# Kernel optimization log

Hardware: AMD Instinct MI355X
Metric: run time of the kernel (lower is better)

## Reference

```python
import jax, jax.numpy as jnp
import numpy as np

B, L, DM, NL, ED, NS, DC, RK, CD, Q = 8, 1024, 256, 4, 512, 16, 4, 16, 64, 2


def _ln(x, g, b, eps=1e-5):
    m = x.mean(-1, keepdims=True)
    v = ((x - m) ** 2).mean(-1, keepdims=True)
    return (x - m) / jnp.sqrt(v + eps) * g + b


def setup_inputs() -> dict:
    key = jax.random.key(0)
    ks = jax.random.split(key, 32)
    rn = lambda k, sh, s=0.02: jax.random.normal(k, sh, jnp.float32) * s
    inp = {
        "tokens": jax.random.randint(ks[0], (B, L), 0, Q),
        "T": jax.random.uniform(ks[1], (B,), jnp.float32, 0.5, 2.0),
        "tok_embed": rn(ks[2], (Q, DM)),
        "pos_embed": rn(ks[3], (L, DM)),
        "tw1": rn(ks[4], (1, CD), 0.5),
        "tb1": rn(ks[5], (CD,), 0.1),
        "tw2": rn(ks[6], (CD, CD), 0.1),
        "tb2": rn(ks[7], (CD,), 0.1),
        "ag": jnp.ones((NL, DM), jnp.float32),
        "ab": jnp.zeros((NL, DM), jnp.float32),
        "apw": rn(ks[8], (NL, CD, 2 * DM), 0.01),
        "apb": jnp.zeros((NL, 2 * DM), jnp.float32),
        "in_w": rn(ks[9], (NL, DM, 2 * ED)),
        "conv_w": rn(ks[10], (NL, ED, DC), 0.2),
        "conv_b": jnp.zeros((NL, ED), jnp.float32),
        "xp_w": rn(ks[11], (NL, ED, RK + 2 * NS)),
        "dt_w": rn(ks[12], (NL, RK, ED), 0.1),
        "dt_b": rn(ks[13], (NL, ED), 0.1) - 4.0,  # softplus(~-4) gives small dt
        "A_log": jnp.log(jnp.broadcast_to(jnp.arange(1, NS + 1, dtype=jnp.float32), (NL, ED, NS))),
        "Dp": jnp.ones((NL, ED), jnp.float32),
        "out_w": rn(ks[14], (NL, ED, DM)),
        "fg": jnp.ones((DM,), jnp.float32),
        "fb": jnp.zeros((DM,), jnp.float32),
        "hw": rn(ks[15], (DM, Q)),
        "hb": jnp.zeros((Q,), jnp.float32),
    }
    return inp


def reference(tokens, T, tok_embed, pos_embed, tw1, tb1, tw2, tb2, ag, ab, apw, apb,
              in_w, conv_w, conv_b, xp_w, dt_w, dt_b, A_log, Dp, out_w, fg, fb, hw, hb):
    b, l = tokens.shape
    # shift-right token embedding + positional embedding
    emb = tok_embed[tokens]                                   # [B,L,DM]
    x = jnp.concatenate([jnp.zeros((b, 1, emb.shape[-1]), emb.dtype), emb[:, :-1]], axis=1)
    x = x + pos_embed[:l]
    # temperature conditioning MLP (exact GELU as in torch nn.GELU)
    h = jax.nn.gelu(T[:, None] @ tw1 + tb1, approximate=False)
    cond = h @ tw2 + tb2                                      # [B,CD]

    def comb(e1, e2):
        a1, b1 = e1
        a2, b2 = e2
        return a1 * a2, a2 * b1 + b2

    for i in range(NL):
        # AdaLN: (1 + scale) * LN(x) + shift
        ss = cond @ apw[i] + apb[i]                           # [B,2*DM]
        sc, sh = ss[:, :DM], ss[:, DM:]
        xn = (1.0 + sc[:, None, :]) * _ln(x, ag[i], ab[i]) + sh[:, None, :]
        # MambaBlock
        xz = xn @ in_w[i]                                     # [B,L,2*ED]
        xs, z = xz[..., :ED], xz[..., ED:]
        # causal depthwise conv1d (left-pad d_conv-1)
        xc = jnp.transpose(xs, (0, 2, 1))                     # [B,ED,L]
        xc = jax.lax.conv_general_dilated(xc, conv_w[i][:, None, :], (1,), [(DC - 1, 0)],
                                          feature_group_count=ED)
        xc = xc + conv_b[i][None, :, None]
        xs = jax.nn.silu(jnp.transpose(xc, (0, 2, 1)))        # [B,L,ED]
        # input-dependent SSM params
        xd = xs @ xp_w[i]                                     # [B,L,RK+2*NS]
        dlt = jax.nn.softplus(xd[..., :RK] @ dt_w[i] + dt_b[i])  # [B,L,ED]
        Bm, Cm = xd[..., RK:RK + NS], xd[..., RK + NS:]       # [B,L,NS]
        A = -jnp.exp(A_log[i])                                # [ED,NS]
        dA = jnp.exp(dlt[..., None] * A)                      # [B,L,ED,NS]
        dBx = (dlt * xs)[..., None] * Bm[:, :, None, :]       # [B,L,ED,NS]
        # selective scan: h_t = dA_t * h_{t-1} + dBx_t (parallel associative scan)
        _, hs = jax.lax.associative_scan(comb, (dA, dBx), axis=1)
        y = jnp.einsum('blen,bln->ble', hs, Cm) + Dp[i] * xs
        y = y * jax.nn.silu(z)
        x = x + y @ out_w[i]

    x = _ln(x, fg, fb)
    return x @ hw + hb                                        # [B,L,Q]
```

## Files before the change

### kernel.cpp

```cpp
#include <hip/hip_runtime.h>
#include <hip/hip_bf16.h>
#include <math.h>

#define B_   8
#define L_   1024
#define DM_  256
#define NL_  4
#define ED_  512
#define NS_  16
#define DC_  4
#define RK_  16
#define CD_  64
#define Q_   2

#define SEG_  32
#define SLEN_ 32

typedef __hip_bfloat16 bf16_t;
typedef __attribute__((ext_vector_type(8))) short short8;
typedef __attribute__((ext_vector_type(4))) float floatx4;

__device__ __forceinline__ float geluf(float x) {
    return 0.5f * x * (1.0f + erff(x * 0.70710678118654752f));
}
__device__ __forceinline__ float siluf(float x) {
    return x / (1.0f + __expf(-x));
}
__device__ __forceinline__ float softplusf(float x) {
    return (x > 20.0f) ? x : log1pf(expf(x));
}
__device__ __forceinline__ float b2f(bf16_t v) { return __bfloat162float(v); }
__device__ __forceinline__ short f2bfbits(float v) {
    return __builtin_bit_cast(short, __float2bfloat16(v));
}

__global__ void k_transpose_all(const float* __restrict__ in_w,
                                const float* __restrict__ xp_w,
                                const float* __restrict__ out_w,
                                bf16_t* __restrict__ in_wT,
                                bf16_t* __restrict__ xp_wT,
                                bf16_t* __restrict__ out_wT) {
    __shared__ float t[32][33];
    int z = blockIdx.z;
    int which = z >> 2, layer = z & 3;
    const float* src; bf16_t* dst; int R, C;
    if (which == 0)      { R = DM_; C = 2 * ED_; src = in_w;  dst = in_wT;  }
    else if (which == 1) { R = ED_; C = 48;      src = xp_w;  dst = xp_wT;  }
    else                 { R = ED_; C = DM_;     src = out_w; dst = out_wT; }
    src += (size_t)layer * R * C;
    dst += (size_t)layer * R * C;
    int c0 = blockIdx.x * 32, r0 = blockIdx.y * 32;
    if (c0 >= C || r0 >= R) return;
    int tx = threadIdx.x & 31, ty = threadIdx.x >> 5;
    #pragma unroll
    for (int i = 0; i < 32; i += 8) {
        int r = r0 + ty + i, c = c0 + tx;
        t[ty + i][tx] = (r < R && c < C) ? src[(size_t)r * C + c] : 0.f;
    }
    __syncthreads();
    #pragma unroll
    for (int i = 0; i < 32; i += 8) {
        int c = c0 + ty + i, r = r0 + tx;
        if (c < C && r < R) dst[(size_t)c * R + r] = __float2bfloat16(t[tx][ty + i]);
    }
}

__global__ void k_embed(const int* __restrict__ tokens,
                        const float* __restrict__ tok_embed,
                        const float* __restrict__ pos_embed,
                        float* __restrict__ x) {
    int row = blockIdx.x;
    int d = threadIdx.x;
    int b = row / L_, l = row % L_;
    float v = pos_embed[l * DM_ + d];
    if (l > 0) {
        int tok = tokens[b * L_ + l - 1];
        v += tok_embed[tok * DM_ + d];
    }
    x[row * DM_ + d] = v;
}

__global__ void k_prep(const float* __restrict__ T,
                       const float* __restrict__ tw1, const float* __restrict__ tb1,
                       const float* __restrict__ tw2, const float* __restrict__ tb2,
                       const float* __restrict__ apw, const float* __restrict__ apb,
                       float* __restrict__ ss) {
    __shared__ float h[CD_], cnd[CD_];
    int b = blockIdx.x, layer = blockIdx.y;
    int j = threadIdx.x;
    if (j < CD_) h[j] = geluf(T[b] * tw1[j] + tb1[j]);
    __syncthreads();
    if (j < CD_) {
        float acc = tb2[j];
        #pragma unroll
        for (int c = 0; c < CD_; c++) acc += h[c] * tw2[c * CD_ + j];
        cnd[j] = acc;
    }
    __syncthreads();
    const float* w = apw + (size_t)layer * CD_ * 2 * DM_;
    float acc = apb[layer * 2 * DM_ + j];
    #pragma unroll
    for (int c = 0; c < CD_; c++) acc += cnd[c] * w[c * 2 * DM_ + j];
    ss[((size_t)layer * B_ + b) * 2 * DM_ + j] = acc;
}

__global__ __launch_bounds__(256) void k_ln_gemm_in(
        const float* __restrict__ x,
        const float* __restrict__ ag, const float* __restrict__ ab,
        const float* __restrict__ ss,
        const bf16_t* __restrict__ Bt,
        bf16_t* __restrict__ xz, int layer) {
    constexpr int BM = 64, BN = 128, K = 256, N = 2 * ED_;
    constexpr int TM = 2, TN = 4;
    __shared__ __align__(16) unsigned short sA[BM * 40];
    __shared__ __align__(16) unsigned short sB[BN * 40];
    __shared__ float s_mr[BM][2];
    __shared__ float s_prm[4 * DM_];

    const int tid = threadIdx.x;
    const int wave = tid >> 6, lane = tid & 63;
    const int lrow = lane & 15, lq = lane >> 4;
    const int bi = blockIdx.x;
    const int row0 = (bi & 127) * BM, col0 = (bi >> 7) * BN;
    const int b = row0 / L_;
    const int wm0 = (wave >> 1) * 32, wn0 = (wave & 1) * 64;

    {
        s_prm[tid]       = ag[layer * DM_ + tid];
        s_prm[256 + tid] = ab[layer * DM_ + tid];
        const float* ssl = ss + ((size_t)layer * B_ + b) * 2 * DM_;
        s_prm[512 + tid] = 1.0f + ssl[tid];
        s_prm[768 + tid] = ssl[DM_ + tid];
    }
    {
        int r = tid >> 2, part = tid & 3;
        const float* xr = x + (size_t)(row0 + r) * K + part * 64;
        float s = 0.f, q = 0.f;
        #pragma unroll
        for (int i = 0; i < 16; i++) {
            float4 v = *(const float4*)(xr + i * 4);
            s += (v.x + v.y) + (v.z + v.w);
            q += (v.x * v.x + v.y * v.y) + (v.z * v.z + v.w * v.w);
        }
        s += __shfl_xor(s, 1, 64);  q += __shfl_xor(q, 1, 64);
        s += __shfl_xor(s, 2, 64);  q += __shfl_xor(q, 2, 64);
        if (part == 0) {
            float mean = s * (1.0f / K);
            float var = q * (1.0f / K) - mean * mean;
            s_mr[r][0] = mean;
            s_mr[r][1] = rsqrtf(var + 1e-5f);
        }
    }

    floatx4 acc[TM][TN];
    #pragma unroll
    for (int i = 0; i < TM; i++)
        #pragma unroll
        for (int j = 0; j < TN; j++) acc[i][j] = (floatx4)0.0f;

    float4 raf[2];
    short8 rb[2];
    const int NKB = K / 32;
    {
        int m = tid >> 2, ko = (tid & 3) * 8;
        raf[0] = *(const float4*)(x + (size_t)(row0 + m) * K + ko);
        raf[1] = *(const float4*)(x + (size_t)(row0 + m) * K + ko + 4);
    }
    #pragma unroll
    for (int i = 0; i < 2; i++) {
        int v = tid + i * 256; int n = v >> 2, ko = (v & 3) * 8;
        rb[i] = *(const short8*)(Bt + (size_t)(col0 + n) * K + ko);
    }

    for (int kb = 0; kb < NKB; kb++) {
        __syncthreads();
        {
            int m = tid >> 2, ko = (tid & 3) * 8;
            int c0 = kb * 32 + ko;
            float mean = s_mr[m][0], rstd = s_mr[m][1];
            float av[8] = {raf[0].x, raf[0].y, raf[0].z, raf[0].w,
                           raf[1].x, raf[1].y, raf[1].z, raf[1].w};
            short8 o;
            #pragma unroll
            for (int j = 0; j < 8; j++) {
                int c = c0 + j;
                float ln = (av[j] - mean) * rstd * s_prm[c] + s_prm[256 + c];
                o[j] = f2bfbits(s_prm[512 + c] * ln + s_prm[768 + c]);
            }
            *(short8*)&sA[m * 40 + ko] = o;
        }
        #pragma unroll
        for (int i = 0; i < 2; i++) {
            int v = tid + i * 256; int n = v >> 2, ko = (v & 3) * 8;
            *(short8*)&sB[n * 40 + ko] = rb[i];
        }
        __syncthreads();
        if (kb + 1 < NKB) {
            int k0 = (kb + 1) * 32;
            {
                int m = tid >> 2, ko = (tid & 3) * 8;
                raf[0] = *(const float4*)(x + (size_t)(row0 + m) * K + k0 + ko);
                raf[1] = *(const float4*)(x + (size_t)(row0 + m) * K + k0 + ko + 4);
            }
            #pragma unroll
            for (int i = 0; i < 2; i++) {
                int v = tid + i * 256; int n = v >> 2, ko = (v & 3) * 8;
                rb[i] = *(const short8*)(Bt + (size_t)(col0 + n) * K + k0 + ko);
            }
        }
        short8 af[TM], bfr[TN];
        #pragma unroll
        for (int i = 0; i < TM; i++)
            af[i] = *(const short8*)&sA[(wm0 + i * 16 + lrow) * 40 + lq * 8];
        #pragma unroll
        for (int j = 0; j < TN; j++)
            bfr[j] = *(const short8*)&sB[(wn0 + j * 16 + lrow) * 40 + lq * 8];
        #pragma unroll
        for (int i = 0; i < TM; i++)
            #pragma unroll
            for (int j = 0; j < TN; j++)
                acc[i][j] = __builtin_amdgcn_mfma_f32_16x16x32_bf16(af[i], bfr[j], acc[i][j], 0, 0, 0);
    }

    #pragma unroll
    for (int i = 0; i < TM; i++) {
        int gr0 = row0 + wm0 + i * 16 + lq * 4;
        #pragma unroll
        for (int j = 0; j < TN; j++) {
            int gc = col0 + wn0 + j * 16 + lrow;
            #pragma unroll
            for (int r = 0; r < 4; r++) {
                float val = acc[i][j][r];
                if (gc >= ED_) val = siluf(val);
                xz[(size_t)(gr0 + r) * N + gc] = __float2bfloat16(val);
            }
        }
    }
}

template<int BM, int BN>
__global__ __launch_bounds__(256) void k_mfma_gemm_acc(
        const bf16_t* __restrict__ A, const bf16_t* __restrict__ Bt,
        float* __restrict__ Cf, int M, int N, int K) {
    constexpr int TM = BM / 32, TN = BN / 32;
    constexpr int VA = BM * 4, VB = BN * 4;
    constexpr int NA = (VA + 255) / 256;
    constexpr int NB = (VB + 255) / 256;
    __shared__ __align__(16) unsigned short sA[BM * 40];
    __shared__ __align__(16) unsigned short sB[BN * 40];

    const int tid = threadIdx.x;
    const int wave = tid >> 6, lane = tid & 63;
    const int lrow = lane & 15, lq = lane >> 4;
    const int nrt = M / BM;
    const int bi = blockIdx.x;
    const int row0 = (bi % nrt) * BM, col0 = (bi / nrt) * BN;
    const int wm0 = (wave >> 1) * (BM / 2);
    const int wn0 = (wave & 1) * (BN / 2);

    floatx4 acc[TM][TN];
    #pragma unroll
    for (int i = 0; i < TM; i++)
        #pragma unroll
        for (int j = 0; j < TN; j++) acc[i][j] = (floatx4)0.0f;

    short8 ra[NA], rb[NB];
    const int NKB = K / 32;

    #pragma unroll
    for (int i = 0; i < NA; i++) {
        int v = tid + i * 256;
        if (v < VA) {
            int m = v >> 2, ko = (v & 3) * 8;
            ra[i] = *(const short8*)(A + (size_t)(row0 + m) * K + ko);
        }
    }
    #pragma unroll
    for (int i = 0; i < NB; i++) {
        int v = tid + i * 256;
        if (v < VB) {
            int n = v >> 2, ko = (v & 3) * 8;
            rb[i] = *(const short8*)(Bt + (size_t)(col0 + n) * K + ko);
        }
    }

    for (int kb = 0; kb < NKB; kb++) {
        __syncthreads();
        #pragma unroll
        for (int i = 0; i < NA; i++) {
            int v = tid + i * 256;
            if (v < VA) {
                int m = v >> 2, ko = (v & 3) * 8;
                *(short8*)&sA[m * 40 + ko] = ra[i];
            }
        }
        #pragma unroll
        for (int i = 0; i < NB; i++) {
            int v = tid + i * 256;
            if (v < VB) {
                int n = v >> 2, ko = (v & 3) * 8;
                *(short8*)&sB[n * 40 + ko] = rb[i];
            }
        }
        __syncthreads();
        if (kb + 1 < NKB) {
            int k0 = (kb + 1) * 32;
            #pragma unroll
            for (int i = 0; i < NA; i++) {
                int v = tid + i * 256;
                if (v < VA) {
                    int m = v >> 2, ko = (v & 3) * 8;
                    ra[i] = *(const short8*)(A + (size_t)(row0 + m) * K + k0 + ko);
                }
            }
            #pragma unroll
            for (int i = 0; i < NB; i++) {
                int v = tid + i * 256;
                if (v < VB) {
                    int n = v >> 2, ko = (v & 3) * 8;
                    rb[i] = *(const short8*)(Bt + (size_t)(col0 + n) * K + k0 + ko);
                }
            }
        }
        short8 af[TM], bfr[TN];
        #pragma unroll
        for (int i = 0; i < TM; i++)
            af[i] = *(const short8*)&sA[(wm0 + i * 16 + lrow) * 40 + lq * 8];
        #pragma unroll
        for (int j = 0; j < TN; j++)
            bfr[j] = *(const short8*)&sB[(wn0 + j * 16 + lrow) * 40 + lq * 8];
        #pragma unroll
        for (int i = 0; i < TM; i++)
            #pragma unroll
            for (int j = 0; j < TN; j++)
                acc[i][j] = __builtin_amdgcn_mfma_f32_16x16x32_bf16(af[i], bfr[j], acc[i][j], 0, 0, 0);
    }

    #pragma unroll
    for (int i = 0; i < TM; i++) {
        int gr0 = row0 + wm0 + i * 16 + lq * 4;
        #pragma unroll
        for (int j = 0; j < TN; j++) {
            int gc = col0 + wn0 + j * 16 + lrow;
            #pragma unroll
            for (int r = 0; r < 4; r++)
                Cf[(size_t)(gr0 + r) * N + gc] += acc[i][j][r];
        }
    }
}

__global__ __launch_bounds__(256) void k_conv_xp_dlt(
        const bf16_t* __restrict__ xz,
        const float* __restrict__ conv_w, const float* __restrict__ conv_b,
        const bf16_t* __restrict__ Bt,
        bf16_t* __restrict__ xs,
        float* __restrict__ xd,
        const float* __restrict__ dt_w, const float* __restrict__ dt_b,
        bf16_t* __restrict__ dlt, int layer) {
    constexpr int K = ED_;
    __shared__ __align__(16) unsigned short sA[32][520];
    __shared__ __align__(16) unsigned short sB[64][520];
    __shared__ float s_rk[32][17];

    const int tid = threadIdx.x;
    const int wave = tid >> 6, lane = tid & 63;
    const int lrow = lane & 15, lq = lane >> 4;
    const int row0 = blockIdx.x * 32;
    const int b = row0 >> 10;
    const int l0 = row0 & (L_ - 1);
    const int wm0 = (wave >> 1) * 16;
    const int wn0 = (wave & 1) * 32;

    #pragma unroll
    for (int i = 0; i < 12; i++) {
        int v = tid + i * 256;
        int n = v >> 6, ko = (v & 63) * 8;
        *(short8*)&sB[n][ko] = *(const short8*)(Bt + (size_t)n * K + ko);
    }
    #pragma unroll
    for (int i = 0; i < 4; i++) {
        int v = tid + i * 256;
        int n = 48 + (v >> 6), ko = (v & 63) * 8;
        *(short8*)&sB[n][ko] = (short8)0;
    }

    {
        const int e0 = tid * 2;
        float4 w0 = *(const float4*)(conv_w + ((size_t)layer * ED_ + e0) * DC_);
        float4 w1 = *(const float4*)(conv_w + ((size_t)layer * ED_ + e0 + 1) * DC_);
        float bias0 = conv_b[layer * ED_ + e0];
        float bias1 = conv_b[layer * ED_ + e0 + 1];
        const float wa0[4] = {w0.x, w0.y, w0.z, w0.w};
        const float wa1[4] = {w1.x, w1.y, w1.z, w1.w};
        float v0[35], v1[35];
        #pragma unroll
        for (int k = 0; k < 35; k++) {
            int ll = l0 - 3 + k;
            if (ll >= 0) {
                __hip_bfloat162 v = *(const __hip_bfloat162*)(
                    xz + ((size_t)(b * L_ + ll)) * (2 * ED_) + e0);
                v0[k] = b2f(v.x); v1[k] = b2f(v.y);
            } else { v0[k] = 0.f; v1[k] = 0.f; }
        }
        #pragma unroll
        for (int j = 0; j < 32; j++) {
            float a0 = bias0, a1 = bias1;
            #pragma unroll
            for (int k = 0; k < DC_; k++) {
                a0 = fmaf(v0[j + k], wa0[k], a0);
                a1 = fmaf(v1[j + k], wa1[k], a1);
            }
            __hip_bfloat162 o;
            o.x = __float2bfloat16(siluf(a0));
            o.y = __float2bfloat16(siluf(a1));
            *(__hip_bfloat162*)(xs + (size_t)(row0 + j) * ED_ + e0) = o;
            *(__hip_bfloat162*)&sA[j][e0] = o;
        }
    }
    __syncthreads();

    floatx4 acc[2];
    acc[0] = (floatx4)0.0f; acc[1] = (floatx4)0.0f;
    #pragma unroll 4
    for (int kb = 0; kb < K / 32; kb++) {
        short8 af = *(const short8*)&sA[wm0 + lrow][kb * 32 + lq * 8];
        short8 b0 = *(const short8*)&sB[wn0 + lrow][kb * 32 + lq * 8];
        short8 b1 = *(const short8*)&sB[wn0 + 16 + lrow][kb * 32 + lq * 8];
        acc[0] = __builtin_amdgcn_mfma_f32_16x16x32_bf16(af, b0, acc[0], 0, 0, 0);
        acc[1] = __builtin_amdgcn_mfma_f32_16x16x32_bf16(af, b1, acc[1], 0, 0, 0);
    }

    #pragma unroll
    for (int j = 0; j < 2; j++) {
        int gc = wn0 + j * 16 + lrow;
        #pragma unroll
        for (int r = 0; r < 4; r++) {
            int gr = row0 + wm0 + lq * 4 + r;
            if (gc >= 16 && gc < 48) xd[(size_t)gr * 48 + gc] = acc[j][r];
        }
    }
    if ((wave & 1) == 0) {
        #pragma unroll
        for (int r = 0; r < 4; r++)
            s_rk[wm0 + lq * 4 + r][lrow] = acc[0][r];
    }
    __syncthreads();

    const int e = 2 * tid;
    float2 wv[16];
    #pragma unroll
    for (int r = 0; r < RK_; r++)
        wv[r] = *(const float2*)(dt_w + ((size_t)layer * RK_ + r) * ED_ + e);
    float2 bb = *(const float2*)(dt_b + (size_t)layer * ED_ + e);
    #pragma unroll 4
    for (int row = 0; row < 32; row++) {
        float a0 = bb.x, a1 = bb.y;
        #pragma unroll
        for (int r = 0; r < RK_; r++) {
            float rk = s_rk[row][r];
            a0 = fmaf(rk, wv[r].x, a0);
            a1 = fmaf(rk, wv[r].y, a1);
        }
        __hip_bfloat162 o;
        o.x = __float2bfloat16(softplusf(a0));
        o.y = __float2bfloat16(softplusf(a1));
        *(__hip_bfloat162*)(dlt + (size_t)(row0 + row) * ED_ + e) = o;
    }
}


__global__ __launch_bounds__(256) void k_scan1(
        const bf16_t* __restrict__ dlt, const bf16_t* __restrict__ xs,
        const float* __restrict__ xd,
        const float* __restrict__ A_log,
        float* __restrict__ aprod, float* __restrict__ hend, int layer) {
    __shared__ float s_B[SLEN_][16];
    const int te = threadIdx.x;
    const int bi = blockIdx.x;
    const int seg = bi & (SEG_ - 1);
    const int eh  = (bi >> 5) & 1;
    const int b   = bi >> 6;
    const int e   = eh * 256 + te;
    const int rowbase = b * L_ + seg * SLEN_;

    if (te < SLEN_ * 4) {
        int flat = te * 4;
        int r = flat >> 4, c = flat & 15;
        *(float4*)&s_B[r][c] = *(const float4*)(xd + (size_t)(rowbase + r) * 48 + 16 + c);
    }

    float A[16];
    bool geo = true;
    {
        const float* ap = A_log + ((size_t)layer * ED_ + e) * NS_;
        #pragma unroll
        for (int n = 0; n < 16; n++) A[n] = -__expf(ap[n]);
        #pragma unroll
        for (int n = 1; n < 16; n++)
            geo = geo && (fabsf(A[n] - (float)(n + 1) * A[0]) <= 1e-3f * (float)(n + 1) * fabsf(A[0]));
    }

    float h[16];
    #pragma unroll
    for (int n = 0; n < 16; n++) h[n] = 0.f;
    float Pr = 1.0f;
    float P[16];
    #pragma unroll
    for (int n = 0; n < 16; n++) P[n] = 1.f;

    const bf16_t* dptr = dlt + (size_t)rowbase * ED_ + e;
    const bf16_t* xptr = xs  + (size_t)rowbase * ED_ + e;

    bf16_t dvb[8], xvb[8];
    #pragma unroll
    for (int j = 0; j < 8; j++) {
        dvb[j] = dptr[(size_t)j * ED_];
        xvb[j] = xptr[(size_t)j * ED_];
    }
    __syncthreads();

    for (int sub = 0; sub < SLEN_ / 8; sub++) {
        bf16_t dnx[8], xnx[8];
        if (sub < SLEN_ / 8 - 1) {
            const bf16_t* d2 = dptr + (size_t)(sub + 1) * 8 * ED_;
            const bf16_t* x2 = xptr + (size_t)(sub + 1) * 8 * ED_;
            #pragma unroll
            for (int j = 0; j < 8; j++) {
                dnx[j] = d2[(size_t)j * ED_];
                xnx[j] = x2[(size_t)j * ED_];
            }
        }
        if (geo) {
            #pragma unroll
            for (int j = 0; j < 8; j++) {
                int l = sub * 8 + j;
                float dv = b2f(dvb[j]), xv = b2f(xvb[j]);
                float dx = dv * xv;
                float Bv[16];
                #pragma unroll
                for (int q = 0; q < 4; q++)
                    *(float4*)&Bv[q * 4] = *(const float4*)&s_B[l][q * 4];
                float r = __expf(dv * A[0]);
                float r2 = r * r, r4 = r2 * r2;
                float a0 = r, a1 = r2, a2 = r2 * r, a3 = r4;
                #pragma unroll
                for (int q = 0; q < 4; q++) {
                    h[4*q+0] = fmaf(a0, h[4*q+0], dx * Bv[4*q+0]);
                    h[4*q+1] = fmaf(a1, h[4*q+1], dx * Bv[4*q+1]);
                    h[4*q+2] = fmaf(a2, h[4*q+2], dx * Bv[4*q+2]);
                    h[4*q+3] = fmaf(a3, h[4*q+3], dx * Bv[4*q+3]);
                    if (q < 3) { a0 *= r4; a1 *= r4; a2 *= r4; a3 *= r4; }
                }
                Pr *= r;
            }
        } else {
            #pragma unroll
            for (int j = 0; j < 8; j++) {
                int l = sub * 8 + j;
                float dv = b2f(dvb[j]), xv = b2f(xvb[j]);
                float dx = dv * xv;
                float Bv[16];
                #pragma unroll
                for (int q = 0; q < 4; q++)
                    *(float4*)&Bv[q * 4] = *(const float4*)&s_B[l][q * 4];
                #pragma unroll
                for (int n = 0; n < 16; n++) {
                    float a = __expf(dv * A[n]);
                    h[n] = fmaf(a, h[n], dx * Bv[n]);
                    P[n] *= a;
                }
            }
        }
        #pragma unroll
        for (int j = 0; j < 8; j++) { dvb[j] = dnx[j]; xvb[j] = xnx[j]; }
    }

    if (geo) {
        float p = Pr;
        #pragma unroll
        for (int n = 0; n < 16; n++) { P[n] = p; p *= Pr; }
    }
    #pragma unroll
    for (int n = 0; n < 16; n++) {
        size_t idx = ((((size_t)b * SEG_ + seg) << 4) + n) * ED_ + e;
        aprod[idx] = P[n];
        hend[idx]  = h[n];
    }
}

__global__ __launch_bounds__(256) void k_hinit(
        const float* __restrict__ aprod, const float* __restrict__ hend,
        float* __restrict__ hinit) {
    const int te = threadIdx.x;
    const int bi = blockIdx.x;
    const int n  = bi & 15;
    const int eh = (bi >> 4) & 1;
    const int b  = bi >> 5;
    const int e  = eh * 256 + te;
    float h = 0.f;
    for (int s = 0; s < SEG_; s++) {
        size_t idx = ((((size_t)b * SEG_ + s) << 4) + n) * ED_ + e;
        hinit[idx] = h;
        h = fmaf(aprod[idx], h, hend[idx]);
    }
}

__global__ __launch_bounds__(256) void k_scan3(
        const bf16_t* __restrict__ dlt, const bf16_t* __restrict__ xs,
        const float* __restrict__ xd,
        const bf16_t* __restrict__ xz,
        const float* __restrict__ A_log, const float* __restrict__ Dp,
        const float* __restrict__ hinit,
        bf16_t* __restrict__ y, int layer) {
    __shared__ float s_BC[SLEN_][32];
    const int te = threadIdx.x;
    const int bi = blockIdx.x;
    const int seg = bi & (SEG_ - 1);
    const int eh  = (bi >> 5) & 1;
    const int b   = bi >> 6;
    const int e   = eh * 256 + te;
    const int rowbase = b * L_ + seg * SLEN_;

    {
        int flat = te * 4;
        int r = flat >> 5, c = flat & 31;
        *(float4*)&s_BC[r][c] = *(const float4*)(xd + (size_t)(rowbase + r) * 48 + 16 + c);
    }

    float A[16];
    bool geo = true;
    {
        const float* ap = A_log + ((size_t)layer * ED_ + e) * NS_;
        #pragma unroll
        for (int n = 0; n < 16; n++) A[n] = -__expf(ap[n]);
        #pragma unroll
        for (int n = 1; n < 16; n++)
            geo = geo && (fabsf(A[n] - (float)(n + 1) * A[0]) <= 1e-3f * (float)(n + 1) * fabsf(A[0]));
    }
    const float D = Dp[layer * ED_ + e];

    float h[16];
    {
        const size_t hb = (((size_t)b * SEG_ + seg) << 4) * ED_ + e;
        #pragma unroll
        for (int n = 0; n < 16; n++) h[n] = hinit[hb + (size_t)n * ED_];
    }

    const bf16_t* dptr = dlt + (size_t)rowbase * ED_ + e;
    const bf16_t* xptr = xs  + (size_t)rowbase * ED_ + e;
    const bf16_t* zptr = xz  + (size_t)rowbase * (2 * ED_) + ED_ + e;
    bf16_t*       yptr = y   + (size_t)rowbase * ED_ + e;

    bf16_t dvb[8], xvb[8], zvb[8];
    #pragma unroll
    for (int j = 0; j < 8; j++) {
        dvb[j] = dptr[(size_t)j * ED_];
        xvb[j] = xptr[(size_t)j * ED_];
        zvb[j] = zptr[(size_t)j * (2 * ED_)];
    }
    __syncthreads();

    for (int sub = 0; sub < SLEN_ / 8; sub++) {
        bf16_t dnx[8], xnx[8], znx[8];
        if (sub < SLEN_ / 8 - 1) {
            const bf16_t* d2 = dptr + (size_t)(sub + 1) * 8 * ED_;
            const bf16_t* x2 = xptr + (size_t)(sub + 1) * 8 * ED_;
            const bf16_t* z2 = zptr + (size_t)(sub + 1) * 8 * (2 * ED_);
            #pragma unroll
            for (int j = 0; j < 8; j++) {
                dnx[j] = d2[(size_t)j * ED_];
                xnx[j] = x2[(size_t)j * ED_];
                znx[j] = z2[(size_t)j * (2 * ED_)];
            }
        }
        if (geo) {
            #pragma unroll
            for (int j = 0; j < 8; j++) {
                int l = sub * 8 + j;
                float dv = b2f(dvb[j]), xv = b2f(xvb[j]);
                float dx = dv * xv;
                float Bv[16], Cv[16];
                #pragma unroll
                for (int q = 0; q < 4; q++) {
                    *(float4*)&Bv[q * 4] = *(const float4*)&s_BC[l][q * 4];
                    *(float4*)&Cv[q * 4] = *(const float4*)&s_BC[l][16 + q * 4];
                }
                float r = __expf(dv * A[0]);
                float r2 = r * r, r4 = r2 * r2;
                float a0 = r, a1 = r2, a2 = r2 * r, a3 = r4;
                float y0 = D * xv, y1 = 0.f, y2 = 0.f, y3 = 0.f;
                #pragma unroll
                for (int q = 0; q < 4; q++) {
                    h[4*q+0] = fmaf(a0, h[4*q+0], dx * Bv[4*q+0]);
                    h[4*q+1] = fmaf(a1, h[4*q+1], dx * Bv[4*q+1]);
                    h[4*q+2] = fmaf(a2, h[4*q+2], dx * Bv[4*q+2]);
                    h[4*q+3] = fmaf(a3, h[4*q+3], dx * Bv[4*q+3]);
                    y0 = fmaf(Cv[4*q+0], h[4*q+0], y0);
                    y1 = fmaf(Cv[4*q+1], h[4*q+1], y1);
                    y2 = fmaf(Cv[4*q+2], h[4*q+2], y2);
                    y3 = fmaf(Cv[4*q+3], h[4*q+3], y3);
                    if (q < 3) { a0 *= r4; a1 *= r4; a2 *= r4; a3 *= r4; }
                }
                float yv = (y0 + y1) + (y2 + y3);
                yptr[(size_t)l * ED_] = __float2bfloat16(yv * b2f(zvb[j]));
            }
        } else {
            #pragma unroll
            for (int j = 0; j < 8; j++) {
                int l = sub * 8 + j;
                float dv = b2f(dvb[j]), xv = b2f(xvb[j]);
                float dx = dv * xv;
                float Bv[16], Cv[16];
                #pragma unroll
                for (int q = 0; q < 4; q++) {
                    *(float4*)&Bv[q * 4] = *(const float4*)&s_BC[l][q * 4];
                    *(float4*)&Cv[q * 4] = *(const float4*)&s_BC[l][16 + q * 4];
                }
                float y0 = D * xv, y1 = 0.f, y2 = 0.f, y3 = 0.f;
                #pragma unroll
                for (int n = 0; n < 16; n++) {
                    float a = __expf(dv * A[n]);
                    h[n] = fmaf(a, h[n], dx * Bv[n]);
                    float t = Cv[n] * h[n];
                    if ((n & 3) == 0) y0 += t;
                    else if ((n & 3) == 1) y1 += t;
                    else if ((n & 3) == 2) y2 += t;
                    else y3 += t;
                }
                float yv = (y0 + y1) + (y2 + y3);
                yptr[(size_t)l * ED_] = __float2bfloat16(yv * b2f(zvb[j]));
            }
        }
        #pragma unroll
        for (int j = 0; j < 8; j++) { dvb[j] = dnx[j]; xvb[j] = xnx[j]; zvb[j] = znx[j]; }
    }
}

__global__ void k_final(const float* __restrict__ x,
                        const float* __restrict__ fg, const float* __restrict__ fb,
                        const float* __restrict__ hw, const float* __restrict__ hb,
                        float* __restrict__ out) {
    int lane = threadIdx.x & 63, w = threadIdx.x >> 6;
    int row = blockIdx.x * 4 + w;
    const float* xr = x + (size_t)row * DM_;
    float v[4];
    #pragma unroll
    for (int k = 0; k < 4; k++) v[k] = xr[lane + 64 * k];
    float s = (v[0] + v[1]) + (v[2] + v[3]);
    float q = (v[0] * v[0] + v[1] * v[1]) + (v[2] * v[2] + v[3] * v[3]);
    #pragma unroll
    for (int off = 32; off > 0; off >>= 1) {
        s += __shfl_xor(s, off, 64);
        q += __shfl_xor(q, off, 64);
    }
    float mean = s * (1.0f / DM_);
    float var = q * (1.0f / DM_) - mean * mean;
    float rstd = rsqrtf(var + 1e-5f);
    float s0 = 0.f, s1 = 0.f;
    #pragma unroll
    for (int k = 0; k < 4; k++) {
        int c = lane + 64 * k;
        float xf = (v[k] - mean) * rstd * fg[c] + fb[c];
        s0 += xf * hw[c * Q_ + 0];
        s1 += xf * hw[c * Q_ + 1];
    }
    #pragma unroll
    for (int off = 32; off > 0; off >>= 1) {
        s0 += __shfl_xor(s0, off, 64);
        s1 += __shfl_xor(s1, off, 64);
    }
    if (lane == 0) {
        out[row * Q_ + 0] = s0 + hb[0];
        out[row * Q_ + 1] = s1 + hb[1];
    }
}

extern "C" void kernel_launch(void* const* d_in, const int* in_sizes, int n_in,
                              void* d_out, int out_size, void* d_ws, size_t ws_size,
                              hipStream_t stream) {
    const int*   tokens    = (const int*)d_in[0];
    const float* T         = (const float*)d_in[1];
    const float* tok_embed = (const float*)d_in[2];
    const float* pos_embed = (const float*)d_in[3];
    const float* tw1       = (const float*)d_in[4];
    const float* tb1       = (const float*)d_in[5];
    const float* tw2       = (const float*)d_in[6];
    const float* tb2       = (const float*)d_in[7];
    const float* ag        = (const float*)d_in[8];
    const float* ab        = (const float*)d_in[9];
    const float* apw       = (const float*)d_in[10];
    const float* apb       = (const float*)d_in[11];
    const float* in_w      = (const float*)d_in[12];
    const float* conv_w    = (const float*)d_in[13];
    const float* conv_b    = (const float*)d_in[14];
    const float* xp_w      = (const float*)d_in[15];
    const float* dt_w      = (const float*)d_in[16];
    const float* dt_b      = (const float*)d_in[17];
    const float* A_log     = (const float*)d_in[18];
    const float* Dp        = (const float*)d_in[19];
    const float* out_w     = (const float*)d_in[20];
    const float* fg        = (const float*)d_in[21];
    const float* fb        = (const float*)d_in[22];
    const float* hw        = (const float*)d_in[23];
    const float* hb        = (const float*)d_in[24];
    float* out = (float*)d_out;

    const int ROWS = B_ * L_;

    char* p = (char*)d_ws;
    float*  x      = (float*)p;   p += (size_t)ROWS * DM_ * 4;
    bf16_t* xz     = (bf16_t*)p;  p += (size_t)ROWS * 2 * ED_ * 2;
    bf16_t* xs     = (bf16_t*)p;  p += (size_t)ROWS * ED_ * 2;
    float*  xd     = (float*)p;   p += (size_t)ROWS * 48 * 4;
    bf16_t* dlt    = (bf16_t*)p;  p += (size_t)ROWS * ED_ * 2;
    bf16_t* y      = (bf16_t*)p;  p += (size_t)ROWS * ED_ * 2;
    float*  ss     = (float*)p;   p += (size_t)NL_ * B_ * 2 * DM_ * 4;
    float*  aprod  = (float*)p;   p += (size_t)B_ * SEG_ * NS_ * ED_ * 4;
    float*  hendb  = (float*)p;   p += (size_t)B_ * SEG_ * NS_ * ED_ * 4;
    float*  hinit  = (float*)p;   p += (size_t)B_ * SEG_ * NS_ * ED_ * 4;
    bf16_t* in_wT  = (bf16_t*)p;  p += (size_t)NL_ * 2 * ED_ * DM_ * 2;
    bf16_t* xp_wT  = (bf16_t*)p;  p += (size_t)NL_ * 48 * ED_ * 2;
    bf16_t* out_wT = (bf16_t*)p;  p += (size_t)NL_ * DM_ * ED_ * 2;

    k_transpose_all<<<dim3(32, 16, 12), 256, 0, stream>>>(
        in_w, xp_w, out_w, in_wT, xp_wT, out_wT);
    k_prep<<<dim3(B_, NL_), 2 * DM_, 0, stream>>>(T, tw1, tb1, tw2, tb2, apw, apb, ss);
    k_embed<<<ROWS, DM_, 0, stream>>>(tokens, tok_embed, pos_embed, x);

    for (int i = 0; i < NL_; i++) {
        k_ln_gemm_in<<<1024, 256, 0, stream>>>(
            x, ag, ab, ss, in_wT + (size_t)i * 2 * ED_ * DM_, xz, i);
        k_conv_xp_dlt<<<ROWS / 32, 256, 0, stream>>>(
            xz, conv_w, conv_b, xp_wT + (size_t)i * 48 * ED_, xs, xd,
            dt_w, dt_b, dlt, i);
        k_scan1<<<B_ * 2 * SEG_, 256, 0, stream>>>(dlt, xs, xd, A_log, aprod, hendb, i);
        k_hinit<<<B_ * 2 * NS_, 256, 0, stream>>>(aprod, hendb, hinit);
        k_scan3<<<B_ * 2 * SEG_, 256, 0, stream>>>(
            dlt, xs, xd, xz, A_log, Dp, hinit, y, i);
        k_mfma_gemm_acc<64, 64><<<512, 256, 0, stream>>>(
            y, out_wT + (size_t)i * DM_ * ED_, x, ROWS, DM_, ED_);
    }

    k_final<<<ROWS / 4, 256, 0, stream>>>(x, fg, fb, hw, hb, out);
}
```

Measured before the change: 516.2 us.

## Shrink conv/xp/dlt tile to 16 rows and read xp weights directly from global

```diff
diff --git a/kernel.cpp b/kernel.cpp
--- a/kernel.cpp
+++ b/kernel.cpp
@@ -28,6 +28,9 @@
 }
 __device__ __forceinline__ float softplusf(float x) {
     return (x > 20.0f) ? x : log1pf(expf(x));
+}
+__device__ __forceinline__ float softplus_fast(float x) {
+    return (x > 20.0f) ? x : __logf(1.0f + __expf(x));
 }
 __device__ __forceinline__ float b2f(bf16_t v) { return __bfloat162float(v); }
 __device__ __forceinline__ short f2bfbits(float v) {
@@ -358,31 +361,16 @@
         const float* __restrict__ dt_w, const float* __restrict__ dt_b,
         bf16_t* __restrict__ dlt, int layer) {
     constexpr int K = ED_;
-    __shared__ __align__(16) unsigned short sA[32][520];
-    __shared__ __align__(16) unsigned short sB[64][520];
-    __shared__ float s_rk[32][17];
+    constexpr int BM = 16;
+    __shared__ __align__(16) unsigned short sA[BM][520];
+    __shared__ __align__(16) float s_rk[BM][20];
 
     const int tid = threadIdx.x;
     const int wave = tid >> 6, lane = tid & 63;
     const int lrow = lane & 15, lq = lane >> 4;
-    const int row0 = blockIdx.x * 32;
+    const int row0 = blockIdx.x * BM;
     const int b = row0 >> 10;
     const int l0 = row0 & (L_ - 1);
-    const int wm0 = (wave >> 1) * 16;
-    const int wn0 = (wave & 1) * 32;
-
-    #pragma unroll
-    for (int i = 0; i < 12; i++) {
-        int v = tid + i * 256;
-        int n = v >> 6, ko = (v & 63) * 8;
-        *(short8*)&sB[n][ko] = *(const short8*)(Bt + (size_t)n * K + ko);
-    }
-    #pragma unroll
-    for (int i = 0; i < 4; i++) {
-        int v = tid + i * 256;
-        int n = 48 + (v >> 6), ko = (v & 63) * 8;
-        *(short8*)&sB[n][ko] = (short8)0;
-    }
 
     {
         const int e0 = tid * 2;
@@ -392,9 +380,9 @@
         float bias1 = conv_b[layer * ED_ + e0 + 1];
         const float wa0[4] = {w0.x, w0.y, w0.z, w0.w};
         const float wa1[4] = {w1.x, w1.y, w1.z, w1.w};
-        float v0[35], v1[35];
-        #pragma unroll
-        for (int k = 0; k < 35; k++) {
+        float v0[BM + 3], v1[BM + 3];
+        #pragma unroll
+        for (int k = 0; k < BM + 3; k++) {
             int ll = l0 - 3 + k;
             if (ll >= 0) {
                 __hip_bfloat162 v = *(const __hip_bfloat162*)(
@@ -403,7 +391,7 @@
             } else { v0[k] = 0.f; v1[k] = 0.f; }
         }
         #pragma unroll
-        for (int j = 0; j < 32; j++) {
+        for (int j = 0; j < BM; j++) {
             float a0 = bias0, a1 = bias1;
             #pragma unroll
             for (int k = 0; k < DC_; k++) {
@@ -419,30 +407,28 @@
     }
     __syncthreads();
 
-    floatx4 acc[2];
-    acc[0] = (floatx4)0.0f; acc[1] = (floatx4)0.0f;
-    #pragma unroll 4
+    const int nrow = (wave < 3) ? (wave * 16 + lrow) : lrow;
+    const bf16_t* bptr = Bt + (size_t)nrow * K + lq * 8;
+    floatx4 acc = (floatx4)0.0f;
+    #pragma unroll
     for (int kb = 0; kb < K / 32; kb++) {
-        short8 af = *(const short8*)&sA[wm0 + lrow][kb * 32 + lq * 8];
-        short8 b0 = *(const short8*)&sB[wn0 + lrow][kb * 32 + lq * 8];
-        short8 b1 = *(const short8*)&sB[wn0 + 16 + lrow][kb * 32 + lq * 8];
-        acc[0] = __builtin_amdgcn_mfma_f32_16x16x32_bf16(af, b0, acc[0], 0, 0, 0);
-        acc[1] = __builtin_amdgcn_mfma_f32_16x16x32_bf16(af, b1, acc[1], 0, 0, 0);
-    }
-
-    #pragma unroll
-    for (int j = 0; j < 2; j++) {
-        int gc = wn0 + j * 16 + lrow;
+        short8 af = *(const short8*)&sA[lrow][kb * 32 + lq * 8];
+        short8 bf = *(const short8*)(bptr + kb * 32);
+        acc = __builtin_amdgcn_mfma_f32_16x16x32_bf16(af, bf, acc, 0, 0, 0);
+    }
+
+    if (wave == 1 || wave == 2) {
+        int gc = wave * 16 + lrow;
         #pragma unroll
         for (int r = 0; r < 4; r++) {
-            int gr = row0 + wm0 + lq * 4 + r;
-            if (gc >= 16 && gc < 48) xd[(size_t)gr * 48 + gc] = acc[j][r];
-        }
-    }
-    if ((wave & 1) == 0) {
+            int gr = row0 + lq * 4 + r;
+            xd[(size_t)gr * 48 + gc] = acc[r];
+        }
+    }
+    if (wave == 0) {
         #pragma unroll
         for (int r = 0; r < 4; r++)
-            s_rk[wm0 + lq * 4 + r][lrow] = acc[0][r];
+            s_rk[lq * 4 + r][lrow] = acc[r];
     }
     __syncthreads();
 
@@ -453,17 +439,20 @@
         wv[r] = *(const float2*)(dt_w + ((size_t)layer * RK_ + r) * ED_ + e);
     float2 bb = *(const float2*)(dt_b + (size_t)layer * ED_ + e);
     #pragma unroll 4
-    for (int row = 0; row < 32; row++) {
+    for (int row = 0; row < BM; row++) {
+        float rk[16];
+        #pragma unroll
+        for (int q = 0; q < 4; q++)
+            *(float4*)&rk[q * 4] = *(const float4*)&s_rk[row][q * 4];
         float a0 = bb.x, a1 = bb.y;
         #pragma unroll
         for (int r = 0; r < RK_; r++) {
-            float rk = s_rk[row][r];
-            a0 = fmaf(rk, wv[r].x, a0);
-            a1 = fmaf(rk, wv[r].y, a1);
+            a0 = fmaf(rk[r], wv[r].x, a0);
+            a1 = fmaf(rk[r], wv[r].y, a1);
         }
         __hip_bfloat162 o;
-        o.x = __float2bfloat16(softplusf(a0));
-        o.y = __float2bfloat16(softplusf(a1));
+        o.x = __float2bfloat16(softplus_fast(a0));
+        o.y = __float2bfloat16(softplus_fast(a1));
         *(__hip_bfloat162*)(dlt + (size_t)(row0 + row) * ED_ + e) = o;
     }
 }
@@ -830,7 +819,7 @@
     for (int i = 0; i < NL_; i++) {
         k_ln_gemm_in<<<1024, 256, 0, stream>>>(
             x, ag, ab, ss, in_wT + (size_t)i * 2 * ED_ * DM_, xz, i);
-        k_conv_xp_dlt<<<ROWS / 32, 256, 0, stream>>>(
+        k_conv_xp_dlt<<<ROWS / 16, 256, 0, stream>>>(
             xz, conv_w, conv_b, xp_wT + (size_t)i * 48 * ED_, xs, xd,
             dt_w, dt_b, dlt, i);
         k_scan1<<<B_ * 2 * SEG_, 256, 0, stream>>>(dlt, xs, xd, A_log, aprod, hendb, i);
```

Result: faster. 450.7 us (-12.7%).
